# Kernel tuning notes

Hardware: AMD Instinct MI355X
Metric: run time of the kernel (lower is better)

Reference implementation:

```python
import math
import jax, jax.numpy as jnp
import numpy as np

B, L, CIN, COUT = 128, 100, 55, 55
D, H, DFF, MODES = 512, 8, 512, 32
E = D // H
KERNELS = (12, 24)
NK = len(KERNELS)


def _pos_emb(length, d):
    pos = np.arange(length)[:, None].astype(np.float32)
    div = np.exp(np.arange(0, d, 2).astype(np.float32) * (-math.log(10000.0) / d))
    pe = np.zeros((length, d), dtype=np.float32)
    pe[:, 0::2] = np.sin(pos * div)
    pe[:, 1::2] = np.cos(pos * div)
    return jnp.asarray(pe)


def _circ_conv3(x, W):
    # Conv1d(kernel=3, padding=1, padding_mode='circular', bias=False); x:(B,L,C) W:(O,C,3)
    n = x.shape[1]
    xp = jnp.concatenate([x[:, -1:], x, x[:, :1]], axis=1)
    return (jnp.einsum('blc,oc->blo', xp[:, 0:n], W[:, :, 0]) +
            jnp.einsum('blc,oc->blo', xp[:, 1:n + 1], W[:, :, 1]) +
            jnp.einsum('blc,oc->blo', xp[:, 2:n + 2], W[:, :, 2]))


def _moving_avg(x, k):
    # replicate-pad then length-preserving mean filter (Autoformer moving_avg)
    front = jnp.repeat(x[:, :1], (k - 1) // 2, axis=1)
    end = jnp.repeat(x[:, -1:], k // 2, axis=1)
    xp = jnp.concatenate([front, x, end], axis=1)
    c = jnp.cumsum(xp, axis=1)
    c = jnp.concatenate([jnp.zeros_like(c[:, :1]), c], axis=1)
    return (c[:, k:] - c[:, :-k]) / float(k)


def _decomp(x, w, b):
    # series_decomp_multi with learned softmax mixing (Linear(1, NK))
    means = jnp.stack([_moving_avg(x, k) for k in KERNELS], axis=-1)  # (B,L,D,NK)
    mix = jax.nn.softmax(x[..., None] * w + b, axis=-1)
    mean = jnp.sum(means * mix, axis=-1)
    return x - mean, mean


def _my_layernorm(x, g, b):
    mu = x.mean(-1, keepdims=True)
    var = ((x - mu) ** 2).mean(-1, keepdims=True)
    xh = (x - mu) / jnp.sqrt(var + 1e-5) * g + b
    return xh - xh.mean(axis=1, keepdims=True)


def _fourier_block(q, Wc):
    # q:(B,L,H,E) -> rfft over L, per-mode complex GEMM with Wc:(H,E,E,MODES), irfft
    x = jnp.transpose(q, (0, 2, 3, 1))  # (B,H,E,L)
    xf = jnp.fft.rfft(x, axis=-1)
    sel = jnp.einsum('bhem,heom->bhom', xf[..., :MODES], Wc)
    nfreq = x.shape[-1] // 2 + 1
    out_ft = jnp.zeros(sel.shape[:-1] + (nfreq,), sel.dtype).at[..., :MODES].set(sel)
    out = jnp.fft.irfft(out_ft, n=x.shape[-1], axis=-1)
    return jnp.transpose(out, (0, 3, 1, 2))  # (B,L,H,E)


def _fourier_cross(q, k, Wc):
    # FourierCrossAttention: frequency-domain q*k attention with tanh activation, values = k
    xq = jnp.transpose(q, (0, 2, 3, 1))
    xk = jnp.transpose(k, (0, 2, 3, 1))
    qf = jnp.fft.rfft(xq, axis=-1)[..., :MODES]
    kf = jnp.fft.rfft(xk, axis=-1)[..., :MODES]
    qk = jnp.tanh(jnp.einsum('bhex,bhey->bhxy', qf, kf))
    qkv = jnp.einsum('bhxy,bhey->bhex', qk, kf)
    w = jnp.einsum('bhex,heox->bhox', qkv, Wc)
    nfreq = xq.shape[-1] // 2 + 1
    out_ft = jnp.zeros(w.shape[:-1] + (nfreq,), w.dtype).at[..., :MODES].set(w)
    out = jnp.fft.irfft(out_ft / float(D * D), n=xq.shape[-1], axis=-1)
    return jnp.transpose(out, (0, 3, 1, 2))


def _heads(x, W, b):
    y = x @ W.T + b
    return y.reshape(y.shape[0], y.shape[1], H, E)


def _gelu(x):
    return jax.nn.gelu(x, approximate=False)


def _forward(x, emb_enc_w, emb_dec_w, enc_proj_w, enc_proj_b, enc_sig_w, enc_sig_b,
             enc_four_wr, enc_four_wi, enc_ffn_w1, enc_ffn_w2, enc_dcmp_w, enc_dcmp_b,
             enc_norm_g, enc_norm_b, dec_proj_w, dec_proj_b, dec_four_wr, dec_four_wi,
             crs_proj_w, crs_proj_b, crs_four_wr, crs_four_wi, dec_ffn_w1, dec_ffn_w2,
             dec_dcmp_w, dec_dcmp_b, dec_trend_w, dec_norm_g, dec_norm_b,
             out_proj_w, out_proj_b):
    b, n, _ = x.shape
    dist = jnp.abs(jnp.arange(n)[:, None] - jnp.arange(n)[None, :]).astype(x.dtype)
    # seasonal-trend init decomposition
    trend_init = jnp.broadcast_to(x.mean(axis=1, keepdims=True), x.shape)
    seasonal_init = x - trend_init
    pe = _pos_emb(n, D)
    enc_four = enc_four_wr + 1j * enc_four_wi
    enc = _circ_conv3(x, emb_enc_w) + pe
    series_l, prior_l, sigma_l = [], [], []
    for i in range(enc_proj_w.shape[0]):  # e_layers (structurally distinct params)
        Wp, bp = enc_proj_w[i], enc_proj_b[i]
        q = _heads(enc, Wp[0], bp[0])
        k = _heads(enc, Wp[1], bp[1])
        v = _heads(enc, Wp[2], bp[2])  # projected but unused by FourierBlock (faithful)
        attn_out = _fourier_block(q, enc_four).reshape(b, n, D) @ Wp[3].T + bp[3]
        # Anomaly-Transformer association: series = softmax(QK^T/sqrt(E)), prior = Gaussian kernel
        scores = jnp.einsum('blhe,bshe->bhls', q, k) / math.sqrt(E)
        series = jax.nn.softmax(scores, axis=-1)
        sig = jnp.transpose(enc @ enc_sig_w[i].T + enc_sig_b[i], (0, 2, 1))  # (B,H,L)
        sig = jnp.power(3.0, jax.nn.sigmoid(5.0 * sig) + 1e-5) - 1.0
        prior = jnp.exp(-dist ** 2 / (2.0 * sig[..., None] ** 2)) / (math.sqrt(2.0 * math.pi) * sig[..., None])
        series_l.append(series); prior_l.append(prior); sigma_l.append(sig)
        h = enc + attn_out
        h, _ = _decomp(h, enc_dcmp_w[i, 0], enc_dcmp_b[i, 0])
        y = _gelu(h @ enc_ffn_w1[i].T) @ enc_ffn_w2[i].T
        enc, _ = _decomp(h + y, enc_dcmp_w[i, 1], enc_dcmp_b[i, 1])
    enc = _my_layernorm(enc, enc_norm_g, enc_norm_b)

    # decoder (d_layers = 1)
    dec = _circ_conv3(seasonal_init, emb_dec_w) + pe
    dec_four = dec_four_wr + 1j * dec_four_wi
    crs_four = crs_four_wr + 1j * crs_four_wi
    q = _heads(dec, dec_proj_w[0], dec_proj_b[0])
    sa = _fourier_block(q, dec_four).reshape(b, n, D) @ dec_proj_w[3].T + dec_proj_b[3]
    h = dec + sa
    h, t1 = _decomp(h, dec_dcmp_w[0], dec_dcmp_b[0])
    qc = _heads(h, crs_proj_w[0], crs_proj_b[0])
    kc = _heads(enc, crs_proj_w[1], crs_proj_b[1])
    ca = _fourier_cross(qc, kc, crs_four).reshape(b, n, D) @ crs_proj_w[3].T + crs_proj_b[3]
    h = h + ca
    h, t2 = _decomp(h, dec_dcmp_w[1], dec_dcmp_b[1])
    y = _gelu(h @ dec_ffn_w1.T) @ dec_ffn_w2.T
    h, t3 = _decomp(h + y, dec_dcmp_w[2], dec_dcmp_b[2])
    residual_trend = _circ_conv3(t1 + t2 + t3, dec_trend_w)  # (B,L,COUT)
    trend = trend_init + residual_trend
    h = _my_layernorm(h, dec_norm_g, dec_norm_b)
    seasonal = h @ out_proj_w.T + out_proj_b
    dec_out = trend + seasonal
    return dec_out, jnp.stack(series_l), jnp.stack(prior_l), jnp.stack(sigma_l)


def setup_inputs() -> dict:
    key = jax.random.key(0)
    ks = iter(jax.random.split(key, 64))

    def rn(shape, s=0.02):
        return s * jax.random.normal(next(ks), shape, dtype=jnp.float32)

    return dict(
        x=jax.random.normal(next(ks), (B, L, CIN), dtype=jnp.float32),
        emb_enc_w=rn((D, CIN, 3)), emb_dec_w=rn((D, CIN, 3)),
        enc_proj_w=rn((2, 4, D, D)), enc_proj_b=jnp.zeros((2, 4, D), jnp.float32),
        enc_sig_w=rn((2, H, D)), enc_sig_b=jnp.zeros((2, H), jnp.float32),
        enc_four_wr=rn((H, E, E, MODES)), enc_four_wi=rn((H, E, E, MODES)),
        enc_ffn_w1=rn((2, DFF, D)), enc_ffn_w2=rn((2, D, DFF)),
        enc_dcmp_w=rn((2, 2, NK), 1.0), enc_dcmp_b=jnp.zeros((2, 2, NK), jnp.float32),
        enc_norm_g=jnp.ones((D,), jnp.float32), enc_norm_b=jnp.zeros((D,), jnp.float32),
        dec_proj_w=rn((4, D, D)), dec_proj_b=jnp.zeros((4, D), jnp.float32),
        dec_four_wr=rn((H, E, E, MODES)), dec_four_wi=rn((H, E, E, MODES)),
        crs_proj_w=rn((4, D, D)), crs_proj_b=jnp.zeros((4, D), jnp.float32),
        crs_four_wr=rn((H, E, E, MODES)), crs_four_wi=rn((H, E, E, MODES)),
        dec_ffn_w1=rn((DFF, D)), dec_ffn_w2=rn((D, DFF)),
        dec_dcmp_w=rn((3, NK), 1.0), dec_dcmp_b=jnp.zeros((3, NK), jnp.float32),
        dec_trend_w=rn((COUT, D, 3)),
        dec_norm_g=jnp.ones((D,), jnp.float32), dec_norm_b=jnp.zeros((D,), jnp.float32),
        out_proj_w=rn((COUT, D)), out_proj_b=jnp.zeros((COUT,), jnp.float32),
    )


def reference(x, emb_enc_w, emb_dec_w, enc_proj_w, enc_proj_b, enc_sig_w, enc_sig_b,
              enc_four_wr, enc_four_wi, enc_ffn_w1, enc_ffn_w2, enc_dcmp_w, enc_dcmp_b,
              enc_norm_g, enc_norm_b, dec_proj_w, dec_proj_b, dec_four_wr, dec_four_wi,
              crs_proj_w, crs_proj_b, crs_four_wr, crs_four_wi, dec_ffn_w1, dec_ffn_w2,
              dec_dcmp_w, dec_dcmp_b, dec_trend_w, dec_norm_g, dec_norm_b,
              out_proj_w, out_proj_b):
    return _forward(x, emb_enc_w, emb_dec_w, enc_proj_w, enc_proj_b, enc_sig_w, enc_sig_b,
                    enc_four_wr, enc_four_wi, enc_ffn_w1, enc_ffn_w2, enc_dcmp_w, enc_dcmp_b,
                    enc_norm_g, enc_norm_b, dec_proj_w, dec_proj_b, dec_four_wr, dec_four_wi,
                    crs_proj_w, crs_proj_b, crs_four_wr, crs_four_wi, dec_ffn_w1, dec_ffn_w2,
                    dec_dcmp_w, dec_dcmp_b, dec_trend_w, dec_norm_g, dec_norm_b,
                    out_proj_w, out_proj_b)
```

## Files before the change

kernel.cpp:

```cpp
#include <hip/hip_runtime.h>
#include <hip/hip_bf16.h>
#include <cmath>

constexpr int B = 128, L = 100, CIN = 55, COUT = 55;
constexpr int D = 512, H = 8, DFF = 512, MODES = 32, E = 64;
constexpr int NK = 2;
constexpr int M_ROWS = B * L;
constexpr int KEMB = 192;
constexpr size_t BLD  = (size_t)B * L * D;
constexpr size_t BHEM = (size_t)B * H * E * MODES;
constexpr size_t BHLL = (size_t)B * H * L * L;
constexpr float INV_SQRT_2PI = 0.3989422804014327f;

static inline int cdiv(int a, int b) { return (a + b - 1) / b; }

typedef short shortx8 __attribute__((ext_vector_type(8)));
typedef float f32x4 __attribute__((ext_vector_type(4)));

__device__ inline unsigned short f2bf(float f)
{
    unsigned int u = __float_as_uint(f);
    unsigned int r = (u + 0x7FFFu + ((u >> 16) & 1u)) >> 16;
    return (unsigned short)r;
}
__device__ inline unsigned short f2bf_n(float f)
{
    union { __hip_bfloat16 h; unsigned short u; } cv;
    cv.h = __float2bfloat16(f);
    return cv.u;
}
__device__ inline float bf2f(unsigned short u)
{
    union { unsigned int i; float f; } c;
    c.i = (unsigned int)u << 16;
    return c.f;
}

__global__ void init_consts(float* __restrict__ pe)
{
    int idx = blockIdx.x * 256 + threadIdx.x;
    if (idx < L * D) {
        int l = idx / D, d = idx % D;
        int i2 = d & ~1;
        float div = expf((float)i2 * (-logf(10000.f) / (float)D));
        float ang = (float)l * div;
        pe[idx] = (d & 1) ? cosf(ang) : sinf(ang);
    }
}

__global__ void init_tw(unsigned short* __restrict__ twf, unsigned short* __restrict__ twi)
{
    int idx = blockIdx.x * 256 + threadIdx.x;
    if (idx >= 64 * 128) return;
    {
        int mp = idx / 128, t = idx % 128;
        float v = 0.f;
        if (t < L) {
            if (mp < 32) v = cosf(2.f * 3.14159265358979323846f * (float)mp * (float)t / (float)L);
            else v = -sinf(2.f * 3.14159265358979323846f * (float)(mp - 32) * (float)t / (float)L);
        }
        twf[idx] = f2bf(v);
    }
    {
        int t = idx / 64, mp = idx % 64;
        float v = 0.f;
        if (t < L) {
            if (mp == 0) v = 1.f;
            else if (mp < 32) v = 2.f * cosf(2.f * 3.14159265358979323846f * (float)mp * (float)t / (float)L);
            else if (mp == 32) v = 0.f;
            else v = -2.f * sinf(2.f * 3.14159265358979323846f * (float)(mp - 32) * (float)t / (float)L);
        }
        twi[idx] = f2bf(v);
    }
}

__global__ void xmean_kernel(const float* __restrict__ x, float* __restrict__ xm)
{
    int idx = blockIdx.x * 256 + threadIdx.x;
    if (idx >= B * CIN) return;
    int b = idx / CIN, c = idx % CIN;
    float s = 0.f;
    for (int l = 0; l < L; ++l) s += x[((size_t)b * L + l) * CIN + c];
    xm[idx] = s * (1.f / (float)L);
}

struct PrepArgs {
    const float* src[7];
    unsigned short* dst[7];
    int n4[7];
    const float* emb_enc; const float* emb_dec; const float* trend_w; const float* seas_w;
    unsigned short* d_embenc; unsigned short* d_embdec; unsigned short* d_trd; unsigned short* d_seas;
};
__global__ __launch_bounds__(256) void prep_all(PrepArgs a, int total4, int padTotal)
{
    for (int i = blockIdx.x * 256 + threadIdx.x; i < total4 + padTotal; i += gridDim.x * 256) {
        if (i < total4) {
            int idx = i, s = 0;
            while (idx >= a.n4[s]) { idx -= a.n4[s]; ++s; }
            float4 v = *(const float4*)&a.src[s][(size_t)idx * 4];
            ushort4 h;
            h.x = f2bf(v.x); h.y = f2bf(v.y); h.z = f2bf(v.z); h.w = f2bf(v.w);
            *(ushort4*)&a.dst[s][(size_t)idx * 4] = h;
            continue;
        }
        int p = i - total4;
        if (p < D * KEMB) {
            int r = p / KEMB, k = p % KEMB;
            a.d_embenc[p] = (k < CIN * 3) ? f2bf(a.emb_enc[(size_t)r * (CIN * 3) + k]) : (unsigned short)0;
        } else if ((p -= D * KEMB) < D * KEMB) {
            int r = p / KEMB, k = p % KEMB;
            a.d_embdec[p] = (k < CIN * 3) ? f2bf(a.emb_dec[(size_t)r * (CIN * 3) + k]) : (unsigned short)0;
        } else if ((p -= D * KEMB) < 192 * D) {
            int n = p / D, d = p % D;
            int j = n / 64, o = n % 64;
            a.d_trd[p] = (o < COUT) ? f2bf(a.trend_w[(size_t)o * (D * 3) + d * 3 + j]) : (unsigned short)0;
        } else {
            p -= 192 * D;
            int r = p / D, k = p % D;
            a.d_seas[p] = (r < COUT) ? f2bf(a.seas_w[(size_t)r * D + k]) : (unsigned short)0;
        }
    }
}

__global__ __launch_bounds__(256) void transpose_wb(const float* __restrict__ wr, const float* __restrict__ wi,
                                                    unsigned short* __restrict__ wt)
{
    int h = blockIdx.x / E, o = blockIdx.x % E;
    __shared__ float tr[64][33], ti[64][33];
    for (int i = threadIdx.x; i < E * MODES; i += 256) {
        int e = i >> 5, m = i & 31;
        size_t s = (((size_t)h * E + e) * E + o) * MODES + m;
        tr[e][m] = wr[s]; ti[e][m] = wi[s];
    }
    __syncthreads();
    for (int i = threadIdx.x; i < MODES * E; i += 256) {
        int m = i >> 6, e = i & 63;
        size_t base = ((size_t)(h * MODES + m) * 2) * 4096 + (size_t)o * 64 + e;
        wt[base] = f2bf(tr[e][m]);
        wt[base + 4096] = f2bf(ti[e][m]);
    }
}

__global__ void im2col_emb(const float* __restrict__ x, const float* __restrict__ xmean,
                           unsigned short* __restrict__ A2)
{
    int idx = blockIdx.x * 256 + threadIdx.x;
    if (idx >= M_ROWS * KEMB) return;
    int k = idx % KEMB, m = idx / KEMB;
    float v = 0.f;
    if (k < CIN * 3) {
        int c = k / 3, j = k % 3;
        int l = m % L, b = m / L;
        int ls = l + j - 1; ls = (ls + L) % L;
        v = x[((size_t)b * L + ls) * CIN + c];
        if (xmean) v -= xmean[(size_t)b * CIN + c];
    }
    A2[idx] = f2bf(v);
}

template<int BN>
__global__ __launch_bounds__(256) void gemm_mfma(const unsigned short* __restrict__ A,
                                                 const unsigned short* __restrict__ Wb,
                                                 const float* __restrict__ bias, const float* __restrict__ pe,
                                                 float* __restrict__ C, unsigned short* __restrict__ Cb,
                                                 int Nout, int K, int act, int accum)
{
    constexpr int NI = BN / 32;
    constexpr int BI = BN / 64;
    __shared__ unsigned short As[2][128][40];
    __shared__ unsigned short Bs[2][BN][40];
    int tid = threadIdx.x;
    int row0 = blockIdx.y * 128, col0 = blockIdx.x * BN;
    int wid = tid >> 6, lane = tid & 63;
    int wm = wid >> 1, wn = wid & 1;
    int lrow = lane & 15, kg = lane >> 4;
    int ar = tid >> 2, ac8 = (tid & 3) * 8;
    f32x4 acc[4][NI] = {};
    shortx8 rah[2], rbh[BI];

    auto loadG = [&](int k0) {
#pragma unroll
        for (int p = 0; p < 2; ++p)
            rah[p] = *(const shortx8*)&A[(size_t)(row0 + p * 64 + ar) * K + k0 + ac8];
#pragma unroll
        for (int p = 0; p < BI; ++p)
            rbh[p] = *(const shortx8*)&Wb[(size_t)(col0 + p * 64 + ar) * K + k0 + ac8];
    };
    auto storeLDS = [&](int buf) {
#pragma unroll
        for (int p = 0; p < 2; ++p)
            *(shortx8*)&As[buf][p * 64 + ar][ac8] = rah[p];
#pragma unroll
        for (int p = 0; p < BI; ++p)
            *(shortx8*)&Bs[buf][p * 64 + ar][ac8] = rbh[p];
    };

    int nk = K >> 5;
    loadG(0);
    storeLDS(0);
    if (nk > 1) loadG(32);
    __syncthreads();
    int cur = 0;
    for (int s = 0; s < nk; ++s) {
        if (s + 1 < nk) {
            storeLDS(cur ^ 1);
            if (s + 2 < nk) loadG((s + 2) << 5);
        }
        shortx8 av[4], bv[NI];
#pragma unroll
        for (int mi = 0; mi < 4; ++mi)
            av[mi] = *(const shortx8*)&As[cur][wm * 64 + mi * 16 + lrow][kg * 8];
#pragma unroll
        for (int ni = 0; ni < NI; ++ni)
            bv[ni] = *(const shortx8*)&Bs[cur][wn * (BN / 2) + ni * 16 + lrow][kg * 8];
#pragma unroll
        for (int mi = 0; mi < 4; ++mi)
#pragma unroll
            for (int ni = 0; ni < NI; ++ni)
                acc[mi][ni] = __builtin_amdgcn_mfma_f32_16x16x32_bf16(av[mi], bv[ni], acc[mi][ni], 0, 0, 0);
        if (s + 1 < nk) __syncthreads();
        cur ^= 1;
    }
#pragma unroll
    for (int mi = 0; mi < 4; ++mi) {
#pragma unroll
        for (int ni = 0; ni < NI; ++ni) {
            int col = col0 + wn * (BN / 2) + ni * 16 + lrow;
            if (col >= Nout) continue;
#pragma unroll
            for (int r = 0; r < 4; ++r) {
                int row = row0 + wm * 64 + mi * 16 + kg * 4 + r;
                float v = acc[mi][ni][r];
                if (bias) v += bias[col];
                if (pe) v += pe[(size_t)(row % L) * Nout + col];
                if (act) v = 0.5f * v * (1.f + erff(v * 0.70710678118654752f));
                size_t o = (size_t)row * Nout + col;
                if (Cb) Cb[o] = f2bf_n(v);
                else if (accum) C[o] += v;
                else C[o] = v;
            }
        }
    }
}

__global__ __launch_bounds__(256) void scores_softmax(const unsigned short* __restrict__ QK,
                                                      float* __restrict__ out)
{
    int bh = blockIdx.x, b = bh / H, h = bh % H;
    int pass = blockIdx.y;
    __shared__ unsigned short Ks[112][72];
    __shared__ unsigned short Qs[64][72];
    int tid = threadIdx.x;
    int srow = tid >> 4, sc4 = (tid & 15) * 4;
#pragma unroll
    for (int i = 0; i < 7; ++i) {
        int r = i * 16 + srow;
        ushort4 hh = {0, 0, 0, 0};
        if (r < L) hh = *(const ushort4*)&QK[((size_t)b * L + r) * 1024 + 512 + h * E + sc4];
        *(ushort4*)&Ks[r][sc4] = hh;
    }
#pragma unroll
    for (int i = 0; i < 4; ++i) {
        int r = i * 16 + srow;
        int gr = pass * 64 + r;
        ushort4 hh = {0, 0, 0, 0};
        if (gr < L) hh = *(const ushort4*)&QK[((size_t)b * L + gr) * 1024 + h * E + sc4];
        *(ushort4*)&Qs[r][sc4] = hh;
    }
    __syncthreads();
    int wid = tid >> 6, lane = tid & 63;
    int lrow = lane & 15, kg = lane >> 4;
    f32x4 acc[7] = {};
#pragma unroll
    for (int ks = 0; ks < 2; ++ks) {
        shortx8 aq = *(const shortx8*)&Qs[wid * 16 + lrow][ks * 32 + kg * 8];
#pragma unroll
        for (int tj = 0; tj < 7; ++tj) {
            shortx8 bk = *(const shortx8*)&Ks[tj * 16 + lrow][ks * 32 + kg * 8];
            acc[tj] = __builtin_amdgcn_mfma_f32_16x16x32_bf16(aq, bk, acc[tj], 0, 0, 0);
        }
    }
    float mx[4] = {-1e30f, -1e30f, -1e30f, -1e30f};
#pragma unroll
    for (int tj = 0; tj < 7; ++tj) {
        bool valid = (tj * 16 + lrow) < L;
#pragma unroll
        for (int r = 0; r < 4; ++r) {
            float v = acc[tj][r] * 0.125f;
            acc[tj][r] = valid ? v : -1e30f;
            if (valid) mx[r] = fmaxf(mx[r], v);
        }
    }
#pragma unroll
    for (int off = 1; off < 16; off <<= 1)
#pragma unroll
        for (int r = 0; r < 4; ++r) mx[r] = fmaxf(mx[r], __shfl_xor(mx[r], off));
    float sum[4] = {0.f, 0.f, 0.f, 0.f};
#pragma unroll
    for (int tj = 0; tj < 7; ++tj)
#pragma unroll
        for (int r = 0; r < 4; ++r) {
            float e = expf(acc[tj][r] - mx[r]);
            acc[tj][r] = e;
            sum[r] += e;
        }
#pragma unroll
    for (int off = 1; off < 16; off <<= 1)
#pragma unroll
        for (int r = 0; r < 4; ++r) sum[r] += __shfl_xor(sum[r], off);
    float inv[4];
#pragma unroll
    for (int r = 0; r < 4; ++r) inv[r] = 1.f / sum[r];
    float* base = out + (size_t)bh * L * L;
#pragma unroll
    for (int r = 0; r < 4; ++r) {
        int row = pass * 64 + wid * 16 + kg * 4 + r;
        if (row >= L) continue;
#pragma unroll
        for (int tj = 0; tj < 7; ++tj) {
            int col = tj * 16 + lrow;
            if (col < L) base[(size_t)row * L + col] = acc[tj][r] * inv[r];
        }
    }
}

__global__ void trend_combine(const float* __restrict__ Y, const float* __restrict__ xmean,
                              float* __restrict__ dec_out)
{
    int idx = blockIdx.x * 256 + threadIdx.x;
    if (idx >= B * L * COUT) return;
    int o = idx % COUT; int l = (idx / COUT) % L; int b = idx / (COUT * L);
    int lm = (l + L - 1) % L, lp = (l + 1) % L;
    float v = xmean[(size_t)b * CIN + o]
            + Y[((size_t)b * L + lm) * 192 + o]
            + Y[((size_t)b * L + l ) * 192 + 64 + o]
            + Y[((size_t)b * L + lp) * 192 + 128 + o];
    dec_out[idx] = v;
}

__global__ __launch_bounds__(256) void dft_mfma(const unsigned short* __restrict__ X,
                                                const unsigned short* __restrict__ twf,
                                                float2* __restrict__ xf, int stride)
{
    int b = blockIdx.x / H, h = blockIdx.x % H;
    __shared__ unsigned short Xs[64][136];
    int tid = threadIdx.x;
    for (int i = tid; i < L * E / 4; i += 256) {
        int t = i >> 4, e4 = (i & 15) * 4;
        ushort4 u = *(const ushort4*)&X[((size_t)b * L + t) * stride + h * E + e4];
        Xs[e4][t] = u.x; Xs[e4 + 1][t] = u.y; Xs[e4 + 2][t] = u.z; Xs[e4 + 3][t] = u.w;
    }
    for (int i = tid; i < 64 * 28; i += 256) {
        int e = i / 28, t = L + i % 28;
        Xs[e][t] = 0;
    }
    __syncthreads();
    int wid = tid >> 6, lane = tid & 63;
    int lrow = lane & 15, kg = lane >> 4;
    f32x4 acc[4] = {};
#pragma unroll
    for (int k0 = 0; k0 < 4; ++k0) {
        shortx8 bx = *(const shortx8*)&Xs[wid * 16 + lrow][k0 * 32 + kg * 8];
#pragma unroll
        for (int mi = 0; mi < 4; ++mi) {
            shortx8 aw = *(const shortx8*)&twf[(size_t)(mi * 16 + lrow) * 128 + k0 * 32 + kg * 8];
            acc[mi] = __builtin_amdgcn_mfma_f32_16x16x32_bf16(aw, bx, acc[mi], 0, 0, 0);
        }
    }
    int e = wid * 16 + lrow;
#pragma unroll
    for (int mi = 0; mi < 2; ++mi)
#pragma unroll
        for (int r = 0; r < 4; ++r) {
            int m = mi * 16 + kg * 4 + r;
            xf[((size_t)(h * MODES + m) * B + b) * E + e] = make_float2(acc[mi][r], acc[mi + 2][r]);
        }
}

__global__ __launch_bounds__(256) void idft_mfma(const float2* __restrict__ sel,
                                                 const unsigned short* __restrict__ twi,
                                                 unsigned short* __restrict__ out, float scale)
{
    int b = blockIdx.x / H, h = blockIdx.x % H;
    __shared__ unsigned short Ss[64][72];
    int tid = threadIdx.x;
    for (int i = tid; i < MODES * E; i += 256) {
        int m = i >> 6, o = i & 63;
        float2 v = sel[((size_t)(h * MODES + m) * B + b) * E + o];
        Ss[o][m] = f2bf_n(v.x);
        Ss[o][m + 32] = f2bf_n(v.y);
    }
    __syncthreads();
    int wid = tid >> 6, lane = tid & 63;
    int lrow = lane & 15, kg = lane >> 4;
    f32x4 acc[2][4] = {};
#pragma unroll
    for (int k0 = 0; k0 < 2; ++k0) {
        shortx8 bs[4];
#pragma unroll
        for (int ni = 0; ni < 4; ++ni)
            bs[ni] = *(const shortx8*)&Ss[ni * 16 + lrow][k0 * 32 + kg * 8];
#pragma unroll
        for (int ti = 0; ti < 2; ++ti) {
            shortx8 at = *(const shortx8*)&twi[(size_t)((wid * 2 + ti) * 16 + lrow) * 64 + k0 * 32 + kg * 8];
#pragma unroll
            for (int ni = 0; ni < 4; ++ni)
                acc[ti][ni] = __builtin_amdgcn_mfma_f32_16x16x32_bf16(at, bs[ni], acc[ti][ni], 0, 0, 0);
        }
    }
#pragma unroll
    for (int ti = 0; ti < 2; ++ti)
#pragma unroll
        for (int ni = 0; ni < 4; ++ni)
#pragma unroll
            for (int r = 0; r < 4; ++r) {
                int t = (wid * 2 + ti) * 16 + kg * 4 + r;
                if (t < L) {
                    int o = ni * 16 + lrow;
                    out[((size_t)b * L + t) * D + h * E + o] = f2bf_n(acc[ti][ni][r] * scale);
                }
            }
}

__global__ __launch_bounds__(256) void mode_gemm_mfma(float2* __restrict__ xf,
                                                      const unsigned short* __restrict__ wt)
{
    int hm = blockIdx.x;
    int bt = blockIdx.y;
    __shared__ unsigned short XrS[32][72], XiS[32][72];
    __shared__ unsigned short WrS[64][72], WiS[64][72];
    int tid = threadIdx.x;
    for (int i = tid; i < 32 * 64; i += 256) {
        int row = i >> 6, e = i & 63;
        float2 v = xf[((size_t)hm * B + bt * 32 + row) * E + e];
        XrS[row][e] = f2bf_n(v.x);
        XiS[row][e] = f2bf_n(v.y);
    }
    const unsigned short* wr = wt + (size_t)hm * 2 * 4096;
    const unsigned short* wi = wr + 4096;
    for (int i = tid; i < 512; i += 256) {
        int o = i >> 3, e8 = (i & 7) * 8;
        *(shortx8*)&WrS[o][e8] = *(const shortx8*)&wr[(size_t)o * 64 + e8];
        *(shortx8*)&WiS[o][e8] = *(const shortx8*)&wi[(size_t)o * 64 + e8];
    }
    __syncthreads();
    int wid = tid >> 6, lane = tid & 63;
    int lrow = lane & 15, kg = lane >> 4;
    int n0 = wid * 16;
    f32x4 p1[2] = {}, p2[2] = {}, p3[2] = {}, p4[2] = {};
#pragma unroll
    for (int ks = 0; ks < 2; ++ks) {
        shortx8 bR = *(const shortx8*)&WrS[n0 + lrow][ks * 32 + kg * 8];
        shortx8 bI = *(const shortx8*)&WiS[n0 + lrow][ks * 32 + kg * 8];
#pragma unroll
        for (int m = 0; m < 2; ++m) {
            shortx8 aR = *(const shortx8*)&XrS[m * 16 + lrow][ks * 32 + kg * 8];
            shortx8 aI = *(const shortx8*)&XiS[m * 16 + lrow][ks * 32 + kg * 8];
            p1[m] = __builtin_amdgcn_mfma_f32_16x16x32_bf16(aR, bR, p1[m], 0, 0, 0);
            p2[m] = __builtin_amdgcn_mfma_f32_16x16x32_bf16(aI, bI, p2[m], 0, 0, 0);
            p3[m] = __builtin_amdgcn_mfma_f32_16x16x32_bf16(aR, bI, p3[m], 0, 0, 0);
            p4[m] = __builtin_amdgcn_mfma_f32_16x16x32_bf16(aI, bR, p4[m], 0, 0, 0);
        }
    }
    __syncthreads();
#pragma unroll
    for (int m = 0; m < 2; ++m)
#pragma unroll
        for (int r = 0; r < 4; ++r) {
            int row = m * 16 + kg * 4 + r;
            int o = n0 + lrow;
            xf[((size_t)hm * B + bt * 32 + row) * E + o] =
                make_float2(p1[m][r] - p2[m][r], p3[m][r] + p4[m][r]);
        }
}

__global__ __launch_bounds__(256) void fourier_qk_mfma(const float2* __restrict__ qf, float2* __restrict__ kf)
{
    int b = blockIdx.x / H, h = blockIdx.x % H;
    __shared__ unsigned short QR[32][72], QI[32][72], KR[32][72], KI[32][72];
    __shared__ unsigned short KTR[64][40], KTI[64][40];
    __shared__ unsigned short TR[32][40], TI[32][40];
    int tid = threadIdx.x;
    for (int i = tid; i < MODES * E; i += 256) {
        int m = i >> 6, e = i & 63;
        size_t idx = ((size_t)(h * MODES + m) * B + b) * E + e;
        float2 q = qf[idx], k = kf[idx];
        unsigned short kr = f2bf_n(k.x), ki = f2bf_n(k.y);
        QR[m][e] = f2bf_n(q.x); QI[m][e] = f2bf_n(q.y);
        KR[m][e] = kr; KI[m][e] = ki;
        KTR[e][m] = kr; KTI[e][m] = ki;
    }
    __syncthreads();
    int wid = tid >> 6, lane = tid & 63;
    int lrow = lane & 15, kg = lane >> 4;
    {
        int xt = wid >> 1, yt = wid & 1;
        f32x4 p1 = {}, p2 = {}, p3 = {}, p4 = {};
#pragma unroll
        for (int ks = 0; ks < 2; ++ks) {
            shortx8 aR = *(const shortx8*)&QR[xt * 16 + lrow][ks * 32 + kg * 8];
            shortx8 aI = *(const shortx8*)&QI[xt * 16 + lrow][ks * 32 + kg * 8];
            shortx8 bR = *(const shortx8*)&KR[yt * 16 + lrow][ks * 32 + kg * 8];
            shortx8 bI = *(const shortx8*)&KI[yt * 16 + lrow][ks * 32 + kg * 8];
            p1 = __builtin_amdgcn_mfma_f32_16x16x32_bf16(aR, bR, p1, 0, 0, 0);
            p2 = __builtin_amdgcn_mfma_f32_16x16x32_bf16(aI, bI, p2, 0, 0, 0);
            p3 = __builtin_amdgcn_mfma_f32_16x16x32_bf16(aR, bI, p3, 0, 0, 0);
            p4 = __builtin_amdgcn_mfma_f32_16x16x32_bf16(aI, bR, p4, 0, 0, 0);
        }
#pragma unroll
        for (int r = 0; r < 4; ++r) {
            int x = xt * 16 + kg * 4 + r, y = yt * 16 + lrow;
            float re = p1[r] - p2[r], im = p3[r] + p4[r];
            float aa = fminf(fmaxf(2.f * re, -30.f), 30.f);
            float b2 = 2.f * im;
            float den = coshf(aa) + cosf(b2);
            TR[x][y] = f2bf_n(sinhf(aa) / den);
            TI[x][y] = f2bf_n(sinf(b2) / den);
        }
    }
    __syncthreads();
    {
        int xt = wid >> 1;
        shortx8 aR = *(const shortx8*)&TR[xt * 16 + lrow][kg * 8];
        shortx8 aI = *(const shortx8*)&TI[xt * 16 + lrow][kg * 8];
#pragma unroll
        for (int ei = 0; ei < 2; ++ei) {
            int et = (wid & 1) * 2 + ei;
            shortx8 bR = *(const shortx8*)&KTR[et * 16 + lrow][kg * 8];
            shortx8 bI = *(const shortx8*)&KTI[et * 16 + lrow][kg * 8];
            f32x4 p1 = {}, p2 = {}, p3 = {}, p4 = {};
            p1 = __builtin_amdgcn_mfma_f32_16x16x32_bf16(aR, bR, p1, 0, 0, 0);
            p2 = __builtin_amdgcn_mfma_f32_16x16x32_bf16(aI, bI, p2, 0, 0, 0);
            p3 = __builtin_amdgcn_mfma_f32_16x16x32_bf16(aR, bI, p3, 0, 0, 0);
            p4 = __builtin_amdgcn_mfma_f32_16x16x32_bf16(aI, bR, p4, 0, 0, 0);
#pragma unroll
            for (int r = 0; r < 4; ++r) {
                int x = xt * 16 + kg * 4 + r, e = et * 16 + lrow;
                kf[((size_t)(h * MODES + x) * B + b) * E + e] = make_float2(p1[r] - p2[r], p3[r] + p4[r]);
            }
        }
    }
}

__global__ __launch_bounds__(256) void sigma_prior(const unsigned short* __restrict__ enc,
                                                   const float* __restrict__ w,
                                                   const float* __restrict__ bias,
                                                   float* __restrict__ sig_out, float* __restrict__ prior)
{
    __shared__ float wsh[H][D];
    for (int i = threadIdx.x; i < H * D; i += 256) wsh[i / D][i % D] = w[i];
    __syncthreads();
    int wid = threadIdx.x / 64, lane = threadIdx.x % 64;
    int row = blockIdx.x * 4 + wid;
    const unsigned short* p = enc + (size_t)row * D;
    float xv[8];
#pragma unroll
    for (int i = 0; i < 8; ++i) xv[i] = bf2f(p[lane + i * 64]);
    int b = row / L, l = row % L;
#pragma unroll
    for (int h = 0; h < H; ++h) {
        float s = 0.f;
#pragma unroll
        for (int i = 0; i < 8; ++i) s += xv[i] * wsh[h][lane + i * 64];
        for (int off = 32; off; off >>= 1) s += __shfl_xor(s, off);
        float acc = s + bias[h];
        float sg = 1.f / (1.f + expf(-5.f * acc));
        float val = expf((sg + 1e-5f) * 1.0986122886681098f) - 1.f;
        if (lane == 0) sig_out[((size_t)b * H + h) * L + l] = val;
        float inv2 = 1.f / (2.f * val * val);
        float coef = INV_SQRT_2PI / val;
        float* pr = prior + (((size_t)b * H + h) * L + l) * L;
        for (int sc = lane; sc < L; sc += 64) {
            float d = (float)abs(l - sc);
            pr[sc] = expf(-d * d * inv2) * coef;
        }
    }
}

__global__ __launch_bounds__(256) void decomp_kernel(const unsigned short* __restrict__ in1,
                                                     const unsigned short* __restrict__ in2,
                                                     const float* __restrict__ w, const float* __restrict__ bc,
                                                     unsigned short* __restrict__ res, float* __restrict__ trend,
                                                     unsigned short* __restrict__ trend16, int tmode)
{
    int b = blockIdx.x / (D / 64);
    int d0 = (blockIdx.x % (D / 64)) * 64;
    __shared__ float P[125][65];
    __shared__ float qtot[4][64];
    int tid = threadIdx.x;
    int dd = tid & 63, q = tid >> 6;
    int p0 = q * 31;
    float run = 0.f;
#pragma unroll
    for (int i = 0; i < 31; ++i) {
        int p = p0 + i;
        int j = min(max(p - 12, 0), L - 1);
        size_t g = ((size_t)b * L + j) * D + d0 + dd;
        float v = bf2f(in1[g]);
        if (in2) v += bf2f(in2[g]);
        run += v;
        P[p + 1][dd] = run;
    }
    qtot[q][dd] = run;
    if (tid < 64) P[0][dd] = 0.f;
    __syncthreads();
    if (q > 0) {
        float off = qtot[0][dd];
        if (q > 1) off += qtot[1][dd];
        if (q > 2) off += qtot[2][dd];
#pragma unroll
        for (int i = 0; i < 31; ++i)
            P[p0 + i + 1][dd] += off;
    }
    __syncthreads();
    float w0 = w[0], w1 = w[1], b0 = bc[0], b1 = bc[1];
    for (int i = tid; i < L * 64; i += 256) {
        int l = i >> 6, d2 = i & 63;
        float s12 = P[l + 19][d2] - P[l + 7][d2];
        float s24 = P[l + 25][d2] - P[l + 1][d2];
        float x = P[l + 13][d2] - P[l + 12][d2];
        float m0 = s12 * (1.f / 12.f), m1 = s24 * (1.f / 24.f);
        float z0 = x * w0 + b0, z1 = x * w1 + b1;
        float zm = fmaxf(z0, z1);
        float e0 = expf(z0 - zm), e1 = expf(z1 - zm);
        float p0f = e0 / (e0 + e1);
        float mean = m0 * p0f + m1 * (1.f - p0f);
        size_t g = ((size_t)b * L + l) * D + d0 + d2;
        res[g] = f2bf_n(x - mean);
        if (tmode == 1) trend[g] = mean;
        else if (tmode == 2) {
            float tv = trend[g] + mean;
            trend[g] = tv;
            if (trend16) trend16[g] = f2bf_n(tv);
        }
    }
}

__global__ __launch_bounds__(256) void ln_colsub(const unsigned short* __restrict__ x,
                                                 const float* __restrict__ g, const float* __restrict__ bb,
                                                 unsigned short* __restrict__ out)
{
    int b = blockIdx.x;
    __shared__ unsigned short xs[L][D];
    __shared__ float colmean[D];
    __shared__ float gs[D], bs2[D];
    int tid = threadIdx.x;
    for (int i = tid; i < L * D / 8; i += 256) {
        int l = i / 64, c8 = (i % 64) * 8;
        *(shortx8*)&xs[l][c8] = *(const shortx8*)&x[((size_t)b * L + l) * D + c8];
    }
    for (int i = tid; i < D; i += 256) { gs[i] = g[i]; bs2[i] = bb[i]; }
    __syncthreads();
    int wid = tid >> 6, lane = tid & 63;
    for (int l = wid; l < L; l += 4) {
        float v[8];
        float s = 0.f, s2 = 0.f;
#pragma unroll
        for (int i = 0; i < 8; ++i) {
            v[i] = bf2f(xs[l][lane + i * 64]);
            s += v[i]; s2 += v[i] * v[i];
        }
        for (int off = 32; off; off >>= 1) { s += __shfl_xor(s, off); s2 += __shfl_xor(s2, off); }
        float mu = s / (float)D;
        float var = s2 / (float)D - mu * mu;
        float rstd = rsqrtf(var + 1e-5f);
#pragma unroll
        for (int i = 0; i < 8; ++i) {
            int d = lane + i * 64;
            xs[l][d] = f2bf_n((v[i] - mu) * rstd * gs[d] + bs2[d]);
        }
    }
    __syncthreads();
    for (int c = tid; c < D; c += 256) {
        float s = 0.f;
        for (int l = 0; l < L; ++l) s += bf2f(xs[l][c]);
        colmean[c] = s * (1.f / (float)L);
    }
    __syncthreads();
    for (int i = tid; i < L * D; i += 256) {
        int l = i / D, c = i % D;
        out[((size_t)b * L + l) * D + c] = f2bf_n(bf2f(xs[l][c]) - colmean[c]);
    }
}

extern "C" void kernel_launch(void* const* d_in, const int* in_sizes, int n_in,
                              void* d_out, int out_size, void* d_ws, size_t ws_size,
                              hipStream_t stream)
{
    const float* x           = (const float*)d_in[0];
    const float* emb_enc_w   = (const float*)d_in[1];
    const float* emb_dec_w   = (const float*)d_in[2];
    const float* enc_proj_w  = (const float*)d_in[3];
    const float* enc_proj_b  = (const float*)d_in[4];
    const float* enc_sig_w   = (const float*)d_in[5];
    const float* enc_sig_b   = (const float*)d_in[6];
    const float* enc_four_wr = (const float*)d_in[7];
    const float* enc_four_wi = (const float*)d_in[8];
    const float* enc_ffn_w1  = (const float*)d_in[9];
    const float* enc_ffn_w2  = (const float*)d_in[10];
    const float* enc_dcmp_w  = (const float*)d_in[11];
    const float* enc_dcmp_b  = (const float*)d_in[12];
    const float* enc_norm_g  = (const float*)d_in[13];
    const float* enc_norm_b  = (const float*)d_in[14];
    const float* dec_proj_w  = (const float*)d_in[15];
    const float* dec_proj_b  = (const float*)d_in[16];
    const float* dec_four_wr = (const float*)d_in[17];
    const float* dec_four_wi = (const float*)d_in[18];
    const float* crs_proj_w  = (const float*)d_in[19];
    const float* crs_proj_b  = (const float*)d_in[20];
    const float* crs_four_wr = (const float*)d_in[21];
    const float* crs_four_wi = (const float*)d_in[22];
    const float* dec_ffn_w1  = (const float*)d_in[23];
    const float* dec_ffn_w2  = (const float*)d_in[24];
    const float* dec_dcmp_w  = (const float*)d_in[25];
    const float* dec_dcmp_b  = (const float*)d_in[26];
    const float* dec_trend_w = (const float*)d_in[27];
    const float* dec_norm_g  = (const float*)d_in[28];
    const float* dec_norm_b  = (const float*)d_in[29];
    const float* out_proj_w  = (const float*)d_in[30];
    const float* out_proj_b  = (const float*)d_in[31];

    float* ws = (float*)d_ws;
    size_t off = 0;
    float* pe    = ws + off; off += (size_t)L * D;
    float* xmean = ws + off; off += (size_t)B * CIN;
    float* bufF  = ws + off; off += BLD;
    float* tacc  = ws + off; off += BLD;
    float2* xfc  = (float2*)(ws + off); off += 2 * BHEM;
    float2* kfc  = (float2*)(ws + off); off += 2 * BHEM;
    unsigned short* wtbf = (unsigned short*)(ws + off); off += (size_t)H * MODES * 2 * E * E / 2;
    unsigned short* qk16 = (unsigned short*)(ws + off); off += BLD;
    unsigned short* e16  = (unsigned short*)(ws + off); off += BLD / 2;
    unsigned short* c16  = (unsigned short*)(ws + off); off += BLD / 2;
    unsigned short* d16  = (unsigned short*)(ws + off); off += BLD / 2;
    unsigned short* h16  = (unsigned short*)(ws + off); off += BLD / 2;
    unsigned short* t16  = (unsigned short*)(ws + off); off += BLD / 2;
    unsigned short* im16 = (unsigned short*)(ws + off); off += (size_t)M_ROWS * KEMB / 2;
    unsigned short* wbf_encproj = (unsigned short*)(ws + off); off += (size_t)2 * 4 * D * D / 2;
    unsigned short* wbf_ffn1    = (unsigned short*)(ws + off); off += (size_t)2 * DFF * D / 2;
    unsigned short* wbf_ffn2    = (unsigned short*)(ws + off); off += (size_t)2 * D * DFF / 2;
    unsigned short* wbf_decproj = (unsigned short*)(ws + off); off += (size_t)4 * D * D / 2;
    unsigned short* wbf_crsproj = (unsigned short*)(ws + off); off += (size_t)4 * D * D / 2;
    unsigned short* wbf_dffn1   = (unsigned short*)(ws + off); off += (size_t)DFF * D / 2;
    unsigned short* wbf_dffn2   = (unsigned short*)(ws + off); off += (size_t)D * DFF / 2;
    unsigned short* wbf_embenc  = (unsigned short*)(ws + off); off += (size_t)D * KEMB / 2;
    unsigned short* wbf_embdec  = (unsigned short*)(ws + off); off += (size_t)D * KEMB / 2;
    unsigned short* wbf_trd     = (unsigned short*)(ws + off); off += (size_t)192 * D / 2;
    unsigned short* wbf_seas    = (unsigned short*)(ws + off); off += (size_t)64 * D / 2;
    unsigned short* twf         = (unsigned short*)(ws + off); off += (size_t)64 * 128 / 2;
    unsigned short* twi         = (unsigned short*)(ws + off); off += (size_t)128 * 64 / 2;
    unsigned short* a16 = qk16;
    unsigned short* b16 = qk16 + BLD;

    float* out       = (float*)d_out;
    float* dec_out   = out;
    float* series_out= out + (size_t)B * L * COUT;
    float* prior_out = series_out + 2 * BHLL;
    float* sigma_out = prior_out + 2 * BHLL;

    const int BH = B * H;

    init_consts<<<200, 256, 0, stream>>>(pe);
    init_tw<<<32, 256, 0, stream>>>(twf, twi);
    xmean_kernel<<<cdiv(B * CIN, 256), 256, 0, stream>>>(x, xmean);

    PrepArgs pa;
    pa.src[0] = enc_proj_w; pa.dst[0] = wbf_encproj; pa.n4[0] = 2 * 4 * D * D / 4;
    pa.src[1] = enc_ffn_w1; pa.dst[1] = wbf_ffn1;    pa.n4[1] = 2 * DFF * D / 4;
    pa.src[2] = enc_ffn_w2; pa.dst[2] = wbf_ffn2;    pa.n4[2] = 2 * D * DFF / 4;
    pa.src[3] = dec_proj_w; pa.dst[3] = wbf_decproj; pa.n4[3] = 4 * D * D / 4;
    pa.src[4] = crs_proj_w; pa.dst[4] = wbf_crsproj; pa.n4[4] = 4 * D * D / 4;
    pa.src[5] = dec_ffn_w1; pa.dst[5] = wbf_dffn1;   pa.n4[5] = DFF * D / 4;
    pa.src[6] = dec_ffn_w2; pa.dst[6] = wbf_dffn2;   pa.n4[6] = D * DFF / 4;
    pa.emb_enc = emb_enc_w; pa.emb_dec = emb_dec_w; pa.trend_w = dec_trend_w; pa.seas_w = out_proj_w;
    pa.d_embenc = wbf_embenc; pa.d_embdec = wbf_embdec; pa.d_trd = wbf_trd; pa.d_seas = wbf_seas;
    int total4 = 0;
    for (int s = 0; s < 7; ++s) total4 += pa.n4[s];
    int padTotal = 2 * D * KEMB + 192 * D + 64 * D;
    prep_all<<<2048, 256, 0, stream>>>(pa, total4, padTotal);
    transpose_wb<<<H * E, 256, 0, stream>>>(enc_four_wr, enc_four_wi, wtbf);

    auto gemm = [&](const unsigned short* A, const unsigned short* Wb, const float* bias, const float* pe_,
                    float* C, unsigned short* Cb, int N, int Nout, int K, int act, int accum) {
        if (N % 128 == 0) {
            dim3 grid(N / 128, M_ROWS / 128);
            gemm_mfma<128><<<grid, 256, 0, stream>>>(A, Wb, bias, pe_, C, Cb, Nout, K, act, accum);
        } else {
            dim3 grid(N / 64, M_ROWS / 128);
            gemm_mfma<64><<<grid, 256, 0, stream>>>(A, Wb, bias, pe_, C, Cb, Nout, K, act, accum);
        }
    };
    dim3 mg_grid(H * MODES, B / 32);
    dim3 sc_grid(BH, 2);

    im2col_emb<<<cdiv(M_ROWS * KEMB, 256), 256, 0, stream>>>(x, nullptr, im16);
    gemm(im16, wbf_embenc, nullptr, pe, nullptr, e16, D, D, KEMB, 0, 0);

    for (int i = 0; i < 2; ++i) {
        const unsigned short* Wp = wbf_encproj + (size_t)i * 4 * D * D;
        const float* bp = enc_proj_b + (size_t)i * 4 * D;
        float* series_i = series_out + (size_t)i * BHLL;
        float* prior_i  = prior_out  + (size_t)i * BHLL;
        float* sigma_i  = sigma_out  + (size_t)i * B * H * L;

        gemm(e16, Wp, bp, nullptr, nullptr, qk16, 1024, 1024, D, 0, 0);
        dft_mfma<<<BH, 256, 0, stream>>>(qk16, twf, xfc, 1024);
        mode_gemm_mfma<<<mg_grid, 256, 0, stream>>>(xfc, wtbf);
        idft_mfma<<<BH, 256, 0, stream>>>(xfc, twi, c16, 1.f / (float)L);
        gemm(c16, Wp + (size_t)3 * D * D, bp + 3 * D, nullptr, nullptr, d16, D, D, D, 0, 0);
        scores_softmax<<<sc_grid, 256, 0, stream>>>(qk16, series_i);
        sigma_prior<<<M_ROWS / 4, 256, 0, stream>>>(e16, enc_sig_w + (size_t)i * H * D,
                                                    enc_sig_b + (size_t)i * H, sigma_i, prior_i);
        decomp_kernel<<<B * (D / 64), 256, 0, stream>>>(e16, d16, enc_dcmp_w + (size_t)(i * 2 + 0) * NK,
                                                        enc_dcmp_b + (size_t)(i * 2 + 0) * NK, h16, nullptr, nullptr, 0);
        gemm(h16, wbf_ffn1 + (size_t)i * DFF * D, nullptr, nullptr, nullptr, c16, DFF, DFF, D, 1, 0);
        gemm(c16, wbf_ffn2 + (size_t)i * D * DFF, nullptr, nullptr, nullptr, d16, D, D, DFF, 0, 0);
        decomp_kernel<<<B * (D / 64), 256, 0, stream>>>(h16, d16, enc_dcmp_w + (size_t)(i * 2 + 1) * NK,
                                                        enc_dcmp_b + (size_t)(i * 2 + 1) * NK, e16, nullptr, nullptr, 0);
    }
    ln_colsub<<<B, 256, 0, stream>>>(e16, enc_norm_g, enc_norm_b, e16);

    transpose_wb<<<H * E, 256, 0, stream>>>(dec_four_wr, dec_four_wi, wtbf);
    im2col_emb<<<cdiv(M_ROWS * KEMB, 256), 256, 0, stream>>>(x, xmean, im16);
    gemm(im16, wbf_embdec, nullptr, pe, nullptr, a16, D, D, KEMB, 0, 0);
    gemm(a16, wbf_decproj, dec_proj_b, nullptr, nullptr, b16, D, D, D, 0, 0);
    dft_mfma<<<BH, 256, 0, stream>>>(b16, twf, xfc, D);
    mode_gemm_mfma<<<mg_grid, 256, 0, stream>>>(xfc, wtbf);
    idft_mfma<<<BH, 256, 0, stream>>>(xfc, twi, c16, 1.f / (float)L);
    gemm(c16, wbf_decproj + (size_t)3 * D * D, dec_proj_b + 3 * D, nullptr, nullptr, d16, D, D, D, 0, 0);
    decomp_kernel<<<B * (D / 64), 256, 0, stream>>>(a16, d16, dec_dcmp_w, dec_dcmp_b, h16, tacc, nullptr, 1);

    gemm(h16, wbf_crsproj, crs_proj_b, nullptr, nullptr, b16, D, D, D, 0, 0);
    dft_mfma<<<BH, 256, 0, stream>>>(b16, twf, xfc, D);
    gemm(e16, wbf_crsproj + (size_t)D * D, crs_proj_b + D, nullptr, nullptr, b16, D, D, D, 0, 0);
    dft_mfma<<<BH, 256, 0, stream>>>(b16, twf, kfc, D);
    transpose_wb<<<H * E, 256, 0, stream>>>(crs_four_wr, crs_four_wi, wtbf);
    fourier_qk_mfma<<<BH, 256, 0, stream>>>(xfc, kfc);
    mode_gemm_mfma<<<mg_grid, 256, 0, stream>>>(kfc, wtbf);
    idft_mfma<<<BH, 256, 0, stream>>>(kfc, twi, c16, 1.f / ((float)L * (float)D * (float)D));
    gemm(c16, wbf_crsproj + (size_t)3 * D * D, crs_proj_b + 3 * D, nullptr, nullptr, d16, D, D, D, 0, 0);
    decomp_kernel<<<B * (D / 64), 256, 0, stream>>>(h16, d16, dec_dcmp_w + NK, dec_dcmp_b + NK, a16, tacc, nullptr, 2);

    gemm(a16, wbf_dffn1, nullptr, nullptr, nullptr, c16, DFF, DFF, D, 1, 0);
    gemm(c16, wbf_dffn2, nullptr, nullptr, nullptr, d16, D, D, DFF, 0, 0);
    decomp_kernel<<<B * (D / 64), 256, 0, stream>>>(a16, d16, dec_dcmp_w + 2 * NK, dec_dcmp_b + 2 * NK, b16, tacc, t16, 2);

    gemm(t16, wbf_trd, nullptr, nullptr, bufF, nullptr, 192, 192, D, 0, 0);
    trend_combine<<<cdiv(B * L * COUT, 256), 256, 0, stream>>>(bufF, xmean, dec_out);

    ln_colsub<<<B, 256, 0, stream>>>(b16, dec_norm_g, dec_norm_b, d16);
    gemm(d16, wbf_seas, out_proj_b, nullptr, dec_out, nullptr, 64, COUT, D, 0, 1);
}
```

Before: 1.147 ms.

## Stage GEMM tiles with direct global-to-LDS loads and XOR-swizzled layout

The bf16 MFMA GEMM now copies A and B tiles straight from global memory into LDS using global_load_lds, instead of staging them through registers. The LDS layout drops the padded row stride and uses an XOR swizzle on the 16-byte column chunks to avoid bank conflicts. This removes the register round trip and frees VGPRs. The prefetch distance drops from two K-steps (register-held) to one, and every iteration now ends with a barrier.

After: 1.174 ms. +2.4%, slower.

```diff
diff --git a/kernel.cpp b/kernel.cpp
--- a/kernel.cpp
+++ b/kernel.cpp
@@ -34,6 +34,13 @@
     union { unsigned int i; float f; } c;
     c.i = (unsigned int)u << 16;
     return c.f;
+}
+
+__device__ inline void gload16(const unsigned short* g, unsigned short* l)
+{
+    __builtin_amdgcn_global_load_lds(
+        (const __attribute__((address_space(1))) void*)g,
+        (__attribute__((address_space(3))) void*)l, 16, 0, 0);
 }
 
 __global__ void init_consts(float* __restrict__ pe)
@@ -166,59 +173,56 @@
                                                  int Nout, int K, int act, int accum)
 {
     constexpr int NI = BN / 32;
-    constexpr int BI = BN / 64;
-    __shared__ unsigned short As[2][128][40];
-    __shared__ unsigned short Bs[2][BN][40];
+    constexpr int BWI = BN / 64;
+    __shared__ unsigned short As[2][128][32];
+    __shared__ unsigned short Bs[2][BN][32];
     int tid = threadIdx.x;
     int row0 = blockIdx.y * 128, col0 = blockIdx.x * BN;
     int wid = tid >> 6, lane = tid & 63;
     int wm = wid >> 1, wn = wid & 1;
     int lrow = lane & 15, kg = lane >> 4;
-    int ar = tid >> 2, ac8 = (tid & 3) * 8;
     f32x4 acc[4][NI] = {};
-    shortx8 rah[2], rbh[BI];
-
-    auto loadG = [&](int k0) {
-#pragma unroll
-        for (int p = 0; p < 2; ++p)
-            rah[p] = *(const shortx8*)&A[(size_t)(row0 + p * 64 + ar) * K + k0 + ac8];
-#pragma unroll
-        for (int p = 0; p < BI; ++p)
-            rbh[p] = *(const shortx8*)&Wb[(size_t)(col0 + p * 64 + ar) * K + k0 + ac8];
+
+    auto stage = [&](int buf, int k0) {
+#pragma unroll
+        for (int j = 0; j < 2; ++j) {
+            int rbase = wid * 32 + j * 16;
+            int row = rbase + (lane >> 2);
+            int c = (lane & 3) ^ ((row >> 1) & 3);
+            gload16(A + (size_t)(row0 + row) * K + k0 + c * 8, &As[buf][rbase][0]);
+        }
+#pragma unroll
+        for (int j = 0; j < BWI; ++j) {
+            int rbase = wid * (16 * BWI) + j * 16;
+            int row = rbase + (lane >> 2);
+            int c = (lane & 3) ^ ((row >> 1) & 3);
+            gload16(Wb + (size_t)(col0 + row) * K + k0 + c * 8, &Bs[buf][rbase][0]);
+        }
     };
-    auto storeLDS = [&](int buf) {
-#pragma unroll
-        for (int p = 0; p < 2; ++p)
-            *(shortx8*)&As[buf][p * 64 + ar][ac8] = rah[p];
-#pragma unroll
-        for (int p = 0; p < BI; ++p)
-            *(shortx8*)&Bs[buf][p * 64 + ar][ac8] = rbh[p];
-    };
 
     int nk = K >> 5;
-    loadG(0);
-    storeLDS(0);
-    if (nk > 1) loadG(32);
+    stage(0, 0);
     __syncthreads();
     int cur = 0;
     for (int s = 0; s < nk; ++s) {
-        if (s + 1 < nk) {
-            storeLDS(cur ^ 1);
-            if (s + 2 < nk) loadG((s + 2) << 5);
-        }
+        if (s + 1 < nk) stage(cur ^ 1, (s + 1) << 5);
         shortx8 av[4], bv[NI];
 #pragma unroll
-        for (int mi = 0; mi < 4; ++mi)
-            av[mi] = *(const shortx8*)&As[cur][wm * 64 + mi * 16 + lrow][kg * 8];
-#pragma unroll
-        for (int ni = 0; ni < NI; ++ni)
-            bv[ni] = *(const shortx8*)&Bs[cur][wn * (BN / 2) + ni * 16 + lrow][kg * 8];
+        for (int mi = 0; mi < 4; ++mi) {
+            int arow = wm * 64 + mi * 16 + lrow;
+            av[mi] = *(const shortx8*)&As[cur][arow][(kg ^ ((arow >> 1) & 3)) * 8];
+        }
+#pragma unroll
+        for (int ni = 0; ni < NI; ++ni) {
+            int brow = wn * (BN / 2) + ni * 16 + lrow;
+            bv[ni] = *(const shortx8*)&Bs[cur][brow][(kg ^ ((brow >> 1) & 3)) * 8];
+        }
 #pragma unroll
         for (int mi = 0; mi < 4; ++mi)
 #pragma unroll
             for (int ni = 0; ni < NI; ++ni)
                 acc[mi][ni] = __builtin_amdgcn_mfma_f32_16x16x32_bf16(av[mi], bv[ni], acc[mi][ni], 0, 0, 0);
-        if (s + 1 < nk) __syncthreads();
+        __syncthreads();
         cur ^= 1;
     }
 #pragma unroll
```
